# Optimization experiments

Measured on AMD Instinct MI355X. Metric: run time of the kernel, lower is better.

Reference implementation:

```python
import jax, jax.numpy as jnp
import numpy as np


def _slim_scale(out_c, wvec, dtype):
    # SlimConv2d splits output channels at 0.6/0.7/0.8/0.9 and scales splits 1..4
    # by weights[1..4] (split 0 is unscaled). Equivalent to one conv + channel scale.
    c0, c1, c2, c3 = int(0.6 * out_c), int(0.7 * out_c), int(0.8 * out_c), int(0.9 * out_c)
    return jnp.concatenate([
        jnp.ones((c0,), dtype),
        wvec[1] * jnp.ones((c1 - c0,), dtype),
        wvec[2] * jnp.ones((c2 - c1,), dtype),
        wvec[3] * jnp.ones((c3 - c2,), dtype),
        wvec[4] * jnp.ones((out_c - c3,), dtype),
    ])


def _slim_conv(x, W, b, pad_t, wvec):
    # x: (N,C,T,V), W: (O,I,kT,kV)
    y = jax.lax.conv_general_dilated(
        x, W, window_strides=(1, 1), padding=((pad_t, pad_t), (0, 0)),
        dimension_numbers=('NCHW', 'OIHW', 'NCHW'))
    y = y + b[None, :, None, None]
    scale = _slim_scale(W.shape[0], wvec, x.dtype)
    return y * scale[None, :, None, None]


def setup_inputs() -> dict:
    key = jax.random.key(0)
    ks = jax.random.split(key, 8)
    N, C, T, V = 64, 64, 300, 25
    S, IC = 3, 16  # num_subset, inter_channels = 64 // 4
    x = jax.random.normal(ks[0], (N, C, T, V), jnp.float32)
    weights = jax.random.uniform(ks[1], (5,), jnp.float32)
    A = jax.random.uniform(ks[2], (S, V, V), jnp.float32) * 0.1
    PA = jnp.full((S, V, V), 1e-6, jnp.float32)
    Wd = jax.random.normal(ks[3], (S, C, C, 1, 1), jnp.float32) * (2.0 / (C * 3)) ** 0.5
    bd = jnp.zeros((S, C), jnp.float32)
    WT1 = jax.random.normal(ks[4], (S, IC, C, 9, 1), jnp.float32) * 0.05
    bT1 = jnp.zeros((S, IC), jnp.float32)
    WT2 = jax.random.normal(ks[5], (S, IC, C, 9, 1), jnp.float32) * 0.05
    bT2 = jnp.zeros((S, IC), jnp.float32)
    bn_gamma = jnp.ones((C,), jnp.float32)
    bn_beta = jnp.zeros((C,), jnp.float32)
    bn_mean = jnp.zeros((C,), jnp.float32)
    bn_var = jnp.ones((C,), jnp.float32)
    return dict(x=x, weights=weights, A=A, PA=PA, Wd=Wd, bd=bd, WT1=WT1, bT1=bT1,
                WT2=WT2, bT2=bT2, bn_gamma=bn_gamma, bn_beta=bn_beta,
                bn_mean=bn_mean, bn_var=bn_var)


def reference(x, weights, A, PA, Wd, bd, WT1, bT1, WT2, bT2,
              bn_gamma, bn_beta, bn_mean, bn_var):
    N, C, T, V = x.shape
    inter_c = WT1.shape[1]
    num_subset = A.shape[0]
    # Chebyshev-like adjacency term: 8A^4 - 4A^2 - 4A + I (elementwise powers)
    A_ch = 8 * A ** 4 - 4 * A ** 2 - 4 * A + jnp.eye(V, dtype=A.dtype)
    A_full = A + PA + A_ch  # (S, V, V)
    y = None
    for i in range(num_subset):
        t1 = _slim_conv(x, WT1[i], bT1[i], 4, weights)  # (N, inter_c, T, V)
        t2 = _slim_conv(x, WT2[i], bT2[i], 4, weights)  # (N, inter_c, T, V)
        q = t1.transpose(0, 3, 1, 2).reshape(N, V, inter_c * T)  # (N, V, IC*T)
        k = t2.reshape(N, inter_c * T, V)                          # (N, IC*T, V)
        att = jax.nn.softmax(jnp.matmul(q, k) / (inter_c * T), axis=-2)  # (N, V, V)
        A1 = A_full[i] + att
        agg = jnp.matmul(x.reshape(N, C * T, V), A1).reshape(N, C, T, V)
        z = _slim_conv(agg, Wd[i], bd[i], 0, weights)
        y = z if y is None else y + z
    # BatchNorm2d in eval mode
    inv = jax.lax.rsqrt(bn_var + 1e-5)
    y = (y - bn_mean[None, :, None, None]) * (bn_gamma * inv)[None, :, None, None] \
        + bn_beta[None, :, None, None]
    y = y + x  # down is identity since in_channels == out_channels
    return jax.nn.relu(y)
```

## Files before the change

### kernel.cpp

```cpp
#include <hip/hip_runtime.h>

constexpr int N_ = 64, C_ = 64, T_ = 300, V_ = 25, IC_ = 16, S_ = 3, KT_ = 9;

constexpr int TTM   = 16;
constexpr int SROWS = TTM + 8;
constexpr int MROWS = SROWS * V_;
constexpr int CSTR  = 40;
constexpr int NTB   = (T_ + TTM - 1) / TTM;
constexpr int KS_   = 264;

constexpr int TTZ   = 16;
constexpr int NTBZ  = (T_ + TTZ - 1) / TTZ;
constexpr int ASTR  = 36;

typedef __bf16 bf16x8 __attribute__((ext_vector_type(8)));
typedef __bf16 bf16x4 __attribute__((ext_vector_type(4)));
typedef float  f32x4  __attribute__((ext_vector_type(4)));

constexpr int OFF_AFULL = 0;
constexpr int SZ_AFULL  = S_ * V_ * V_;
constexpr int OFF_WTB   = OFF_AFULL + SZ_AFULL;
constexpr int SZ_WTB_F  = (S_ * KT_ * 32 * C_) / 2;
constexpr int OFF_BTC   = OFF_WTB + SZ_WTB_F;
constexpr int OFF_WDB   = OFF_BTC + S_ * 32;
constexpr int SZ_WDB_F  = (S_ * C_ * C_) / 2;
constexpr int OFF_BDT   = OFF_WDB + SZ_WDB_F;
constexpr int OFF_BNA   = OFF_BDT + C_;
constexpr int OFF_BNB   = OFF_BNA + C_;
constexpr int OFF_A1    = OFF_BNB + C_;
constexpr int SZ_A1     = S_ * N_ * V_ * V_;
constexpr int OFF_SPART = OFF_A1 + SZ_A1;
constexpr int SZ_SPART  = S_ * N_ * NTB * V_ * V_;

__device__ __forceinline__ float slim16(const float* w, int o) {
    if (o < 9)  return 1.0f;
    if (o < 11) return w[1];
    if (o < 12) return w[2];
    if (o < 14) return w[3];
    return w[4];
}
__device__ __forceinline__ float slim64(const float* w, int o) {
    if (o < 38) return 1.0f;
    if (o < 44) return w[1];
    if (o < 51) return w[2];
    if (o < 57) return w[3];
    return w[4];
}

__global__ void prep_kernel(const float* __restrict__ wv,  const float* __restrict__ A,
                            const float* __restrict__ PA,  const float* __restrict__ Wd,
                            const float* __restrict__ bd,  const float* __restrict__ WT1,
                            const float* __restrict__ bT1, const float* __restrict__ WT2,
                            const float* __restrict__ bT2, const float* __restrict__ gam,
                            const float* __restrict__ bet, const float* __restrict__ mu,
                            const float* __restrict__ var, float* __restrict__ ws)
{
    const int gid = blockIdx.x * blockDim.x + threadIdx.x;
    const int stride = gridDim.x * blockDim.x;
    for (int idx = gid; idx < S_ * V_ * V_; idx += stride) {
        int uv = idx % (V_ * V_);
        int u = uv / V_, v = uv % V_;
        float a  = A[idx];
        float a2 = a * a;
        ws[OFF_AFULL + idx] = a + PA[idx] + 8.f * a2 * a2 - 4.f * a2 - 4.f * a
                              + (u == v ? 1.f : 0.f);
    }
    {
        __bf16* wtb = (__bf16*)(ws + OFF_WTB);
        for (int idx = gid; idx < S_ * KT_ * 32 * C_; idx += stride) {
            int c  = idx % C_;
            int r  = idx / C_;
            int o  = r % 32;  r /= 32;
            int kt = r % KT_;
            int i  = r / KT_;
            float val;
            if (o < IC_)
                val = slim16(wv, o) * WT1[((i * IC_ + o) * C_ + c) * KT_ + kt];
            else
                val = slim16(wv, o - IC_) * WT2[((i * IC_ + (o - IC_)) * C_ + c) * KT_ + kt];
            wtb[idx] = (__bf16)val;
        }
    }
    for (int idx = gid; idx < S_ * 32; idx += stride) {
        int i = idx / 32, o = idx % 32;
        float val = (o < IC_) ? slim16(wv, o) * bT1[i * IC_ + o]
                              : slim16(wv, o - IC_) * bT2[i * IC_ + (o - IC_)];
        ws[OFF_BTC + idx] = val;
    }
    {
        __bf16* wdb = (__bf16*)(ws + OFF_WDB);
        for (int idx = gid; idx < S_ * C_ * C_; idx += stride) {
            int c = idx % C_;
            int o = (idx / C_) % C_;
            int i = idx / (C_ * C_);
            wdb[idx] = (__bf16)(slim64(wv, o) * Wd[(i * C_ + o) * C_ + c]);
        }
    }
    for (int idx = gid; idx < C_; idx += stride) {
        float bt = 0.f;
        for (int i = 0; i < S_; ++i) bt += slim64(wv, idx) * bd[i * C_ + idx];
        ws[OFF_BDT + idx] = bt;
        float ba = gam[idx] * rsqrtf(var[idx] + 1e-5f);
        ws[OFF_BNA + idx] = ba;
        ws[OFF_BNB + idx] = bet[idx] - mu[idx] * ba;
    }
}

__global__ __launch_bounds__(320) void tconv_att_kernel(
    const float* __restrict__ x,  const __bf16* __restrict__ wt,
    const float* __restrict__ btc, float* __restrict__ spart)
{
    __shared__ __align__(16) char lds_raw[MROWS * CSTR * 2];
    __bf16* xs  = (__bf16*)lds_raw;
    __bf16* t1L = (__bf16*)lds_raw;
    __bf16* t2L = t1L + 32 * KS_;
    const int tid  = threadIdx.x;
    const int n    = blockIdx.y;
    const int tb   = blockIdx.x;
    const int t0   = tb * TTM;
    const int wv   = tid >> 6;
    const int lane = tid & 63;
    const int l15  = lane & 15;
    const int quad = lane >> 4;

    f32x4 acc[5][6];
#pragma unroll
    for (int j = 0; j < 5; ++j)
#pragma unroll
        for (int p = 0; p < 6; ++p) acc[j][p] = (f32x4){0.f, 0.f, 0.f, 0.f};

    for (int ch = 0; ch < 2; ++ch) {
        const int c0 = ch * 32;
        __syncthreads();
        for (int idx = tid; idx < MROWS * 4; idx += 320) {
            const int lr = idx % MROWS;
            const int cg = idx / MROWS;
            const int tg = t0 - 4 + lr / V_;
            bf16x8 pk;
            if (tg >= 0 && tg < T_) {
                const float* gp = x + ((size_t)(n * C_ + c0 + cg * 8) * T_ + (t0 - 4)) * V_ + lr;
#pragma unroll
                for (int jj = 0; jj < 8; ++jj) pk[jj] = (__bf16)gp[(size_t)jj * T_ * V_];
            } else {
#pragma unroll
                for (int jj = 0; jj < 8; ++jj) pk[jj] = (__bf16)0.f;
            }
            *(bf16x8*)&xs[lr * CSTR + cg * 8] = pk;
        }
        __syncthreads();

        for (int kt = 0; kt < KT_; ++kt) {
            bf16x8 a[6];
#pragma unroll
            for (int p = 0; p < 6; ++p) {
                const int i = p >> 1, h = p & 1;
                a[p] = *(const bf16x8*)&wt[((size_t)((i * KT_ + kt) * 32 + h * 16 + l15)) * C_ + c0 + quad * 8];
            }
#pragma unroll
            for (int j = 0; j < 5; ++j) {
                const int r = (wv * 5 + j) * 16 + l15 + V_ * kt;
                const bf16x8 b = *(const bf16x8*)&xs[r * CSTR + quad * 8];
#pragma unroll
                for (int p = 0; p < 6; ++p)
                    acc[j][p] = __builtin_amdgcn_mfma_f32_16x16x32_bf16(a[p], b, acc[j][p], 0, 0, 0);
            }
        }
    }

    for (int i = 0; i < S_; ++i) {
        __syncthreads();
#pragma unroll
        for (int j = 0; j < 5; ++j) {
            const int m  = (wv * 5 + j) * 16 + l15;
            const int tl = m / V_;
            const int u  = m % V_;
            const bool valid = (t0 + tl) < T_;
#pragma unroll
            for (int h = 0; h < 2; ++h) {
                const int p = i * 2 + h;
                __bf16* dst = h ? t2L : t1L;
#pragma unroll
                for (int r = 0; r < 4; ++r) {
                    const int o = quad * 4 + r;
                    const float val = valid ? (acc[j][p][r] + btc[i * 32 + h * 16 + o]) : 0.f;
                    dst[u * KS_ + o * 16 + tl] = (__bf16)val;
                }
            }
        }
        __syncthreads();
        if (wv < 4) {
            const int ut = wv >> 1, vt = wv & 1;
            f32x4 sa = (f32x4){0.f, 0.f, 0.f, 0.f};
#pragma unroll
            for (int ks = 0; ks < 8; ++ks) {
                const bf16x8 A = *(const bf16x8*)&t1L[(ut * 16 + l15) * KS_ + ks * 32 + quad * 8];
                const bf16x8 B = *(const bf16x8*)&t2L[(vt * 16 + l15) * KS_ + ks * 32 + quad * 8];
                sa = __builtin_amdgcn_mfma_f32_16x16x32_bf16(A, B, sa, 0, 0, 0);
            }
            float* sp = spart + (((size_t)i * N_ + n) * NTB + tb) * (V_ * V_);
#pragma unroll
            for (int r = 0; r < 4; ++r) {
                const int u = ut * 16 + quad * 4 + r;
                const int v = vt * 16 + l15;
                if (u < V_ && v < V_) sp[u * V_ + v] = sa[r];
            }
        }
    }
}

__global__ __launch_bounds__(256) void att_softmax_kernel(
    const float* __restrict__ spart, const float* __restrict__ afull,
    float* __restrict__ a1o)
{
    __shared__ float Ss[V_ * V_];
    const int n = blockIdx.x;
    const int i = blockIdx.y;
    const int tid = threadIdx.x;
    for (int p = tid; p < V_ * V_; p += 256) {
        float s = 0.f;
        const float* sp = spart + (((size_t)i * N_ + n) * NTB) * (V_ * V_) + p;
        for (int blk = 0; blk < NTB; ++blk)
            s += sp[(size_t)blk * (V_ * V_)];
        Ss[p] = s * (1.0f / (IC_ * T_));
    }
    __syncthreads();
    if (tid < V_) {
        const int v = tid;
        float m = -1e30f;
#pragma unroll
        for (int u = 0; u < V_; ++u) m = fmaxf(m, Ss[u * V_ + v]);
        float e[V_]; float es = 0.f;
#pragma unroll
        for (int u = 0; u < V_; ++u) { e[u] = expf(Ss[u * V_ + v] - m); es += e[u]; }
        const float inv = 1.0f / es;
#pragma unroll
        for (int u = 0; u < V_; ++u)
            a1o[((size_t)i * N_ + n) * (V_ * V_) + u * V_ + v]
                = afull[i * (V_ * V_) + u * V_ + v] + e[u] * inv;
    }
}

__global__ __launch_bounds__(320) void agg_out_mfma_kernel(
    const float* __restrict__ x,   const float* __restrict__ a1,
    const __bf16* __restrict__ wdb, const float* __restrict__ bdt,
    const float* __restrict__ bna, const float* __restrict__ bnb,
    float* __restrict__ out)
{
    __shared__ __align__(16) __bf16 ags[400 * ASTR];
    __shared__ __align__(16) __bf16 a1t3[S_ * 32 * 32];
    const int tid  = threadIdx.x;
    const int n    = blockIdx.y;
    const int t0   = blockIdx.x * TTZ;
    const int wv   = tid >> 6;
    const int lane = tid & 63;
    const int l15  = lane & 15;
    const int quad = lane >> 4;

    for (int idx = tid; idx < S_ * 1024; idx += 320) {
        const int i = idx >> 10;
        const int r = idx & 1023;
        const int v = r >> 5, u = r & 31;
        float val = (v < V_ && u < V_)
                  ? a1[((size_t)(i * N_ + n) * V_ + u) * V_ + v] : 0.f;
        a1t3[idx] = (__bf16)val;
    }

    f32x4 acc[5][4];
#pragma unroll
    for (int j = 0; j < 5; ++j)
#pragma unroll
        for (int ot = 0; ot < 4; ++ot) acc[j][ot] = (f32x4){0.f, 0.f, 0.f, 0.f};

    const int tg = t0 + l15;
    for (int chunk = 0; chunk < 2; ++chunk) {
        const int c0 = chunk * 32;
        bf16x8 afr[7];
#pragma unroll
        for (int k = 0; k < 7; ++k) {
            const int c = wv + 5 * k;
            bf16x8 pk;
#pragma unroll
            for (int jj = 0; jj < 8; ++jj) pk[jj] = (__bf16)0.f;
            if (c < 32 && tg < T_) {
                const float* gp = x + ((size_t)(n * C_ + c0 + c) * T_ + tg) * V_;
#pragma unroll
                for (int jj = 0; jj < 8; ++jj) {
                    const int u = quad * 8 + jj;
                    if (u < V_) pk[jj] = (__bf16)gp[u];
                }
            }
            afr[k] = pk;
        }
        for (int i = 0; i < S_; ++i) {
            __syncthreads();
            const bf16x8 b0 = *(const bf16x8*)&a1t3[i * 1024 + l15 * 32 + quad * 8];
            const bf16x8 b1 = *(const bf16x8*)&a1t3[i * 1024 + (16 + l15) * 32 + quad * 8];
#pragma unroll
            for (int k = 0; k < 7; ++k) {
                const int c = wv + 5 * k;
                if (c < 32) {
                    f32x4 d0 = (f32x4){0.f, 0.f, 0.f, 0.f};
                    f32x4 d1 = (f32x4){0.f, 0.f, 0.f, 0.f};
                    d0 = __builtin_amdgcn_mfma_f32_16x16x32_bf16(afr[k], b0, d0, 0, 0, 0);
                    d1 = __builtin_amdgcn_mfma_f32_16x16x32_bf16(afr[k], b1, d1, 0, 0, 0);
#pragma unroll
                    for (int r = 0; r < 4; ++r) {
                        const int tl = quad * 4 + r;
                        ags[(tl * V_ + l15) * ASTR + c] = (__bf16)d0[r];
                        if (l15 < V_ - 16)
                            ags[(tl * V_ + 16 + l15) * ASTR + c] = (__bf16)d1[r];
                    }
                }
            }
            __syncthreads();
            bf16x8 bw[4];
#pragma unroll
            for (int ot = 0; ot < 4; ++ot)
                bw[ot] = *(const bf16x8*)&wdb[(size_t)(i * C_ + ot * 16 + l15) * C_ + c0 + quad * 8];
#pragma unroll
            for (int j = 0; j < 5; ++j) {
                const int m2 = (wv * 5 + j) * 16 + l15;
                const bf16x4 lo = *(const bf16x4*)&ags[m2 * ASTR + quad * 8];
                const bf16x4 hi = *(const bf16x4*)&ags[m2 * ASTR + quad * 8 + 4];
                const bf16x8 am = __builtin_shufflevector(lo, hi, 0, 1, 2, 3, 4, 5, 6, 7);
#pragma unroll
                for (int ot = 0; ot < 4; ++ot)
                    acc[j][ot] = __builtin_amdgcn_mfma_f32_16x16x32_bf16(am, bw[ot], acc[j][ot], 0, 0, 0);
            }
        }
    }

    const int mrem = (T_ - t0) * V_;
#pragma unroll
    for (int ot = 0; ot < 4; ++ot) {
        const int o  = ot * 16 + l15;
        const float ba = bna[o], bb = bnb[o], bt = bdt[o];
#pragma unroll
        for (int j = 0; j < 5; ++j) {
            const int m2b = (wv * 5 + j) * 16 + quad * 4;
            if (m2b + 3 < mrem) {
                const size_t gi = (size_t)(n * C_ + o) * (T_ * V_) + (size_t)t0 * V_ + m2b;
                const f32x4 xr = *(const f32x4*)&x[gi];
                f32x4 rs;
#pragma unroll
                for (int r = 0; r < 4; ++r)
                    rs[r] = fmaxf(fmaf(acc[j][ot][r] + bt, ba, bb) + xr[r], 0.f);
                *(f32x4*)&out[gi] = rs;
            }
        }
    }
}

extern "C" void kernel_launch(void* const* d_in, const int* in_sizes, int n_in,
                              void* d_out, int out_size, void* d_ws, size_t ws_size,
                              hipStream_t stream)
{
    (void)in_sizes; (void)n_in; (void)out_size; (void)ws_size;
    const float* x    = (const float*)d_in[0];
    const float* wv   = (const float*)d_in[1];
    const float* A    = (const float*)d_in[2];
    const float* PA   = (const float*)d_in[3];
    const float* Wd   = (const float*)d_in[4];
    const float* bd   = (const float*)d_in[5];
    const float* WT1  = (const float*)d_in[6];
    const float* bT1  = (const float*)d_in[7];
    const float* WT2  = (const float*)d_in[8];
    const float* bT2  = (const float*)d_in[9];
    const float* gam  = (const float*)d_in[10];
    const float* bet  = (const float*)d_in[11];
    const float* mu   = (const float*)d_in[12];
    const float* var  = (const float*)d_in[13];
    float* ws  = (float*)d_ws;
    float* out = (float*)d_out;

    prep_kernel<<<dim3(64), dim3(256), 0, stream>>>(
        wv, A, PA, Wd, bd, WT1, bT1, WT2, bT2, gam, bet, mu, var, ws);

    tconv_att_kernel<<<dim3(NTB, N_), dim3(320), 0, stream>>>(
        x, (const __bf16*)(ws + OFF_WTB), ws + OFF_BTC, ws + OFF_SPART);

    att_softmax_kernel<<<dim3(N_, S_), dim3(256), 0, stream>>>(
        ws + OFF_SPART, ws + OFF_AFULL, ws + OFF_A1);

    agg_out_mfma_kernel<<<dim3(NTBZ, N_), dim3(320), 0, stream>>>(
        x, ws + OFF_A1, (const __bf16*)(ws + OFF_WDB),
        ws + OFF_BDT, ws + OFF_BNA, ws + OFF_BNB, out);
}
```

Baseline: 552.0 us.

## Retile temporal conv to 12 steps with swizzled LDS and atomic score accumulation

Shrinks the time tile of the temporal conv/attention kernel from 16 to 12 so it divides T exactly. This removes padded rows and boundary checks, and 300 tile rows map onto 19 MFMA tiles spread across waves. The LDS channel stride drops to 32 with an XOR swizzle to avoid bank conflicts, and t1/t2 are written as packed 4-element vectors. Per-block partial attention scores are accumulated with global atomicAdd into a zeroed buffer instead of a partial array that softmax reduces later. The trade-off is more blocks and atomic contention, plus an order-dependent floating-point sum.

```diff
diff --git a/kernel.cpp b/kernel.cpp
--- a/kernel.cpp
+++ b/kernel.cpp
@@ -2,12 +2,14 @@
 
 constexpr int N_ = 64, C_ = 64, T_ = 300, V_ = 25, IC_ = 16, S_ = 3, KT_ = 9;
 
-constexpr int TTM   = 16;
+constexpr int TTM   = 12;
 constexpr int SROWS = TTM + 8;
 constexpr int MROWS = SROWS * V_;
-constexpr int CSTR  = 40;
-constexpr int NTB   = (T_ + TTM - 1) / TTM;
-constexpr int KS_   = 264;
+constexpr int XROWS = MROWS + 4;
+constexpr int CSTR  = 32;
+constexpr int NTB   = T_ / TTM;
+constexpr int NTILE = (TTM * V_ + 15) / 16;
+constexpr int KS_   = 204;
 
 constexpr int TTZ   = 16;
 constexpr int NTBZ  = (T_ + TTZ - 1) / TTZ;
@@ -29,8 +31,8 @@
 constexpr int OFF_BNB   = OFF_BNA + C_;
 constexpr int OFF_A1    = OFF_BNB + C_;
 constexpr int SZ_A1     = S_ * N_ * V_ * V_;
-constexpr int OFF_SPART = OFF_A1 + SZ_A1;
-constexpr int SZ_SPART  = S_ * N_ * NTB * V_ * V_;
+constexpr int OFF_SACC  = OFF_A1 + SZ_A1;
+constexpr int SZ_SACC   = S_ * N_ * V_ * V_;
 
 __device__ __forceinline__ float slim16(const float* w, int o) {
     if (o < 9)  return 1.0f;
@@ -57,6 +59,8 @@
 {
     const int gid = blockIdx.x * blockDim.x + threadIdx.x;
     const int stride = gridDim.x * blockDim.x;
+    for (int idx = gid; idx < SZ_SACC; idx += stride)
+        ws[OFF_SACC + idx] = 0.f;
     for (int idx = gid; idx < S_ * V_ * V_; idx += stride) {
         int uv = idx % (V_ * V_);
         int u = uv / V_, v = uv % V_;
@@ -108,24 +112,30 @@
 
 __global__ __launch_bounds__(320) void tconv_att_kernel(
     const float* __restrict__ x,  const __bf16* __restrict__ wt,
-    const float* __restrict__ btc, float* __restrict__ spart)
-{
-    __shared__ __align__(16) char lds_raw[MROWS * CSTR * 2];
+    const float* __restrict__ btc, float* __restrict__ sacc)
+{
+    __shared__ __align__(16) char lds_raw[XROWS * CSTR * 2];
     __bf16* xs  = (__bf16*)lds_raw;
     __bf16* t1L = (__bf16*)lds_raw;
     __bf16* t2L = t1L + 32 * KS_;
     const int tid  = threadIdx.x;
     const int n    = blockIdx.y;
-    const int tb   = blockIdx.x;
-    const int t0   = tb * TTM;
+    const int t0   = blockIdx.x * TTM;
     const int wv   = tid >> 6;
     const int lane = tid & 63;
     const int l15  = lane & 15;
     const int quad = lane >> 4;
 
-    f32x4 acc[5][6];
-#pragma unroll
-    for (int j = 0; j < 5; ++j)
+    if (tid < 16) {
+        bf16x8 z;
+#pragma unroll
+        for (int jj = 0; jj < 8; ++jj) z[jj] = (__bf16)0.f;
+        *(bf16x8*)&xs[(MROWS + (tid >> 2)) * CSTR + (tid & 3) * 8] = z;
+    }
+
+    f32x4 acc[4][6];
+#pragma unroll
+    for (int j = 0; j < 4; ++j)
 #pragma unroll
         for (int p = 0; p < 6; ++p) acc[j][p] = (f32x4){0.f, 0.f, 0.f, 0.f};
 
@@ -145,7 +155,7 @@
 #pragma unroll
                 for (int jj = 0; jj < 8; ++jj) pk[jj] = (__bf16)0.f;
             }
-            *(bf16x8*)&xs[lr * CSTR + cg * 8] = pk;
+            *(bf16x8*)&xs[lr * CSTR + ((cg ^ (lr & 3)) << 3)] = pk;
         }
         __syncthreads();
 
@@ -157,12 +167,15 @@
                 a[p] = *(const bf16x8*)&wt[((size_t)((i * KT_ + kt) * 32 + h * 16 + l15)) * C_ + c0 + quad * 8];
             }
 #pragma unroll
-            for (int j = 0; j < 5; ++j) {
-                const int r = (wv * 5 + j) * 16 + l15 + V_ * kt;
-                const bf16x8 b = *(const bf16x8*)&xs[r * CSTR + quad * 8];
-#pragma unroll
-                for (int p = 0; p < 6; ++p)
-                    acc[j][p] = __builtin_amdgcn_mfma_f32_16x16x32_bf16(a[p], b, acc[j][p], 0, 0, 0);
+            for (int j = 0; j < 4; ++j) {
+                const int jt = wv + 5 * j;
+                if (jt < NTILE) {
+                    const int r = jt * 16 + l15 + V_ * kt;
+                    const bf16x8 b = *(const bf16x8*)&xs[r * CSTR + ((quad ^ (r & 3)) << 3)];
+#pragma unroll
+                    for (int p = 0; p < 6; ++p)
+                        acc[j][p] = __builtin_amdgcn_mfma_f32_16x16x32_bf16(a[p], b, acc[j][p], 0, 0, 0);
+                }
             }
         }
     }
@@ -170,20 +183,22 @@
     for (int i = 0; i < S_; ++i) {
         __syncthreads();
 #pragma unroll
-        for (int j = 0; j < 5; ++j) {
-            const int m  = (wv * 5 + j) * 16 + l15;
-            const int tl = m / V_;
-            const int u  = m % V_;
-            const bool valid = (t0 + tl) < T_;
-#pragma unroll
-            for (int h = 0; h < 2; ++h) {
-                const int p = i * 2 + h;
-                __bf16* dst = h ? t2L : t1L;
-#pragma unroll
-                for (int r = 0; r < 4; ++r) {
-                    const int o = quad * 4 + r;
-                    const float val = valid ? (acc[j][p][r] + btc[i * 32 + h * 16 + o]) : 0.f;
-                    dst[u * KS_ + o * 16 + tl] = (__bf16)val;
+        for (int j = 0; j < 4; ++j) {
+            const int jt = wv + 5 * j;
+            if (jt < NTILE) {
+                const int m = jt * 16 + l15;
+                if (m < TTM * V_) {
+                    const int tl = m / V_;
+                    const int u  = m % V_;
+#pragma unroll
+                    for (int h = 0; h < 2; ++h) {
+                        bf16x4 pk;
+#pragma unroll
+                        for (int r = 0; r < 4; ++r)
+                            pk[r] = (__bf16)(acc[j][i * 2 + h][r] + btc[i * 32 + h * 16 + quad * 4 + r]);
+                        __bf16* dst = (h ? t2L : t1L) + u * KS_ + tl * 16 + quad * 4;
+                        *(bf16x4*)dst = pk;
+                    }
                 }
             }
         }
@@ -192,37 +207,32 @@
             const int ut = wv >> 1, vt = wv & 1;
             f32x4 sa = (f32x4){0.f, 0.f, 0.f, 0.f};
 #pragma unroll
-            for (int ks = 0; ks < 8; ++ks) {
+            for (int ks = 0; ks < 6; ++ks) {
                 const bf16x8 A = *(const bf16x8*)&t1L[(ut * 16 + l15) * KS_ + ks * 32 + quad * 8];
                 const bf16x8 B = *(const bf16x8*)&t2L[(vt * 16 + l15) * KS_ + ks * 32 + quad * 8];
                 sa = __builtin_amdgcn_mfma_f32_16x16x32_bf16(A, B, sa, 0, 0, 0);
             }
-            float* sp = spart + (((size_t)i * N_ + n) * NTB + tb) * (V_ * V_);
+            float* sp = sacc + ((size_t)i * N_ + n) * (V_ * V_);
 #pragma unroll
             for (int r = 0; r < 4; ++r) {
                 const int u = ut * 16 + quad * 4 + r;
                 const int v = vt * 16 + l15;
-                if (u < V_ && v < V_) sp[u * V_ + v] = sa[r];
+                if (u < V_ && v < V_) atomicAdd(&sp[u * V_ + v], sa[r]);
             }
         }
     }
 }
 
 __global__ __launch_bounds__(256) void att_softmax_kernel(
-    const float* __restrict__ spart, const float* __restrict__ afull,
+    const float* __restrict__ sacc, const float* __restrict__ afull,
     float* __restrict__ a1o)
 {
     __shared__ float Ss[V_ * V_];
     const int n = blockIdx.x;
     const int i = blockIdx.y;
     const int tid = threadIdx.x;
-    for (int p = tid; p < V_ * V_; p += 256) {
-        float s = 0.f;
-        const float* sp = spart + (((size_t)i * N_ + n) * NTB) * (V_ * V_) + p;
-        for (int blk = 0; blk < NTB; ++blk)
-            s += sp[(size_t)blk * (V_ * V_)];
-        Ss[p] = s * (1.0f / (IC_ * T_));
-    }
+    for (int p = tid; p < V_ * V_; p += 256)
+        Ss[p] = sacc[((size_t)i * N_ + n) * (V_ * V_) + p] * (1.0f / (IC_ * T_));
     __syncthreads();
     if (tid < V_) {
         const int v = tid;
@@ -377,10 +387,10 @@
         wv, A, PA, Wd, bd, WT1, bT1, WT2, bT2, gam, bet, mu, var, ws);
 
     tconv_att_kernel<<<dim3(NTB, N_), dim3(320), 0, stream>>>(
-        x, (const __bf16*)(ws + OFF_WTB), ws + OFF_BTC, ws + OFF_SPART);
+        x, (const __bf16*)(ws + OFF_WTB), ws + OFF_BTC, ws + OFF_SACC);
 
     att_softmax_kernel<<<dim3(N_, S_), dim3(256), 0, stream>>>(
-        ws + OFF_SPART, ws + OFF_AFULL, ws + OFF_A1);
+        ws + OFF_SACC, ws + OFF_AFULL, ws + OFF_A1);
 
     agg_out_mfma_kernel<<<dim3(NTBZ, N_), dim3(320), 0, stream>>>(
         x, ws + OFF_A1, (const __bf16*)(ws + OFF_WDB),
```

New measurement: 598.2 us. +8.4%, slower.

## Pre-transpose x to padded bf16 channel-last layout and atomically accumulate attention scores

Applied to the files above, without the earlier changes.

Adds a pass in the prep kernel that converts x once into a time-padded, channel-last bf16 tensor, stored in the output buffer as scratch. The temporal-conv kernel can then load its LDS tiles with contiguous 16-byte reads instead of strided fp32 gathers with bounds checks. Per-block attention partials are now summed straight into a small accumulator with float atomics, so the softmax kernel no longer reduces over all time blocks. The t1/t2 LDS writes are packed into bf16x4 stores with a changed layout and padding. Costs are an extra full pass over x, a much larger prep grid, atomic contention, and order-dependent float summation.

```diff
diff --git a/kernel.cpp b/kernel.cpp
--- a/kernel.cpp
+++ b/kernel.cpp
@@ -1,13 +1,15 @@
 #include <hip/hip_runtime.h>
 
 constexpr int N_ = 64, C_ = 64, T_ = 300, V_ = 25, IC_ = 16, S_ = 3, KT_ = 9;
+
+constexpr int TP_   = T_ + 12;
 
 constexpr int TTM   = 16;
 constexpr int SROWS = TTM + 8;
 constexpr int MROWS = SROWS * V_;
-constexpr int CSTR  = 40;
+constexpr int CSTR  = 32;
 constexpr int NTB   = (T_ + TTM - 1) / TTM;
-constexpr int KS_   = 264;
+constexpr int KS_   = 266;
 
 constexpr int TTZ   = 16;
 constexpr int NTBZ  = (T_ + TTZ - 1) / TTZ;
@@ -29,8 +31,8 @@
 constexpr int OFF_BNB   = OFF_BNA + C_;
 constexpr int OFF_A1    = OFF_BNB + C_;
 constexpr int SZ_A1     = S_ * N_ * V_ * V_;
-constexpr int OFF_SPART = OFF_A1 + SZ_A1;
-constexpr int SZ_SPART  = S_ * N_ * NTB * V_ * V_;
+constexpr int OFF_SACC  = OFF_A1 + SZ_A1;
+constexpr int SZ_SACC   = S_ * N_ * V_ * V_;
 
 __device__ __forceinline__ float slim16(const float* w, int o) {
     if (o < 9)  return 1.0f;
@@ -47,7 +49,8 @@
     return w[4];
 }
 
-__global__ void prep_kernel(const float* __restrict__ wv,  const float* __restrict__ A,
+__global__ void prep_kernel(const float* __restrict__ x,   __bf16* __restrict__ xt,
+                            const float* __restrict__ wv,  const float* __restrict__ A,
                             const float* __restrict__ PA,  const float* __restrict__ Wd,
                             const float* __restrict__ bd,  const float* __restrict__ WT1,
                             const float* __restrict__ bT1, const float* __restrict__ WT2,
@@ -57,6 +60,25 @@
 {
     const int gid = blockIdx.x * blockDim.x + threadIdx.x;
     const int stride = gridDim.x * blockDim.x;
+    for (int idx = gid; idx < N_ * TP_ * V_ * 8; idx += stride) {
+        const int cg = idx & 7;
+        const int v  = (idx >> 3) % V_;
+        const int tt = (idx / (V_ * 8)) % TP_;
+        const int n  = idx / (V_ * 8 * TP_);
+        const int t  = tt - 4;
+        bf16x8 pk;
+        if (t >= 0 && t < T_) {
+            const float* gp = x + ((size_t)(n * C_ + cg * 8) * T_ + t) * V_ + v;
+#pragma unroll
+            for (int jj = 0; jj < 8; ++jj) pk[jj] = (__bf16)gp[(size_t)jj * T_ * V_];
+        } else {
+#pragma unroll
+            for (int jj = 0; jj < 8; ++jj) pk[jj] = (__bf16)0.f;
+        }
+        *(bf16x8*)&xt[((size_t)(n * TP_ + tt) * V_ + v) * C_ + cg * 8] = pk;
+    }
+    for (int idx = gid; idx < SZ_SACC; idx += stride)
+        ws[OFF_SACC + idx] = 0.f;
     for (int idx = gid; idx < S_ * V_ * V_; idx += stride) {
         int uv = idx % (V_ * V_);
         int u = uv / V_, v = uv % V_;
@@ -107,8 +129,8 @@
 }
 
 __global__ __launch_bounds__(320) void tconv_att_kernel(
-    const float* __restrict__ x,  const __bf16* __restrict__ wt,
-    const float* __restrict__ btc, float* __restrict__ spart)
+    const __bf16* __restrict__ xt, const __bf16* __restrict__ wt,
+    const float* __restrict__ btc, float* __restrict__ sacc)
 {
     __shared__ __align__(16) char lds_raw[MROWS * CSTR * 2];
     __bf16* xs  = (__bf16*)lds_raw;
@@ -116,8 +138,7 @@
     __bf16* t2L = t1L + 32 * KS_;
     const int tid  = threadIdx.x;
     const int n    = blockIdx.y;
-    const int tb   = blockIdx.x;
-    const int t0   = tb * TTM;
+    const int t0   = blockIdx.x * TTM;
     const int wv   = tid >> 6;
     const int lane = tid & 63;
     const int l15  = lane & 15;
@@ -132,20 +153,13 @@
     for (int ch = 0; ch < 2; ++ch) {
         const int c0 = ch * 32;
         __syncthreads();
-        for (int idx = tid; idx < MROWS * 4; idx += 320) {
-            const int lr = idx % MROWS;
-            const int cg = idx / MROWS;
-            const int tg = t0 - 4 + lr / V_;
-            bf16x8 pk;
-            if (tg >= 0 && tg < T_) {
-                const float* gp = x + ((size_t)(n * C_ + c0 + cg * 8) * T_ + (t0 - 4)) * V_ + lr;
-#pragma unroll
-                for (int jj = 0; jj < 8; ++jj) pk[jj] = (__bf16)gp[(size_t)jj * T_ * V_];
-            } else {
-#pragma unroll
-                for (int jj = 0; jj < 8; ++jj) pk[jj] = (__bf16)0.f;
-            }
-            *(bf16x8*)&xs[lr * CSTR + cg * 8] = pk;
+        {
+            const __bf16* xtb = xt + (size_t)(n * TP_ + t0) * (V_ * C_) + c0;
+            for (int idx = tid; idx < MROWS * 4; idx += 320) {
+                const int lr = idx >> 2, cg = idx & 3;
+                const bf16x8 pk = *(const bf16x8*)&xtb[lr * C_ + cg * 8];
+                *(bf16x8*)&xs[idx * 8] = pk;
+            }
         }
         __syncthreads();
 
@@ -177,14 +191,15 @@
             const bool valid = (t0 + tl) < T_;
 #pragma unroll
             for (int h = 0; h < 2; ++h) {
-                const int p = i * 2 + h;
-                __bf16* dst = h ? t2L : t1L;
+                bf16x4 pk;
 #pragma unroll
                 for (int r = 0; r < 4; ++r) {
-                    const int o = quad * 4 + r;
-                    const float val = valid ? (acc[j][p][r] + btc[i * 32 + h * 16 + o]) : 0.f;
-                    dst[u * KS_ + o * 16 + tl] = (__bf16)val;
+                    const float val = valid
+                        ? (acc[j][i * 2 + h][r] + btc[i * 32 + h * 16 + quad * 4 + r])
+                        : 0.f;
+                    pk[r] = (__bf16)val;
                 }
+                *(bf16x4*)((h ? t2L : t1L) + u * KS_ + tl * 16 + quad * 4) = pk;
             }
         }
         __syncthreads();
@@ -197,32 +212,27 @@
                 const bf16x8 B = *(const bf16x8*)&t2L[(vt * 16 + l15) * KS_ + ks * 32 + quad * 8];
                 sa = __builtin_amdgcn_mfma_f32_16x16x32_bf16(A, B, sa, 0, 0, 0);
             }
-            float* sp = spart + (((size_t)i * N_ + n) * NTB + tb) * (V_ * V_);
+            float* sp = sacc + ((size_t)i * N_ + n) * (V_ * V_);
 #pragma unroll
             for (int r = 0; r < 4; ++r) {
                 const int u = ut * 16 + quad * 4 + r;
                 const int v = vt * 16 + l15;
-                if (u < V_ && v < V_) sp[u * V_ + v] = sa[r];
+                if (u < V_ && v < V_) atomicAdd(&sp[u * V_ + v], sa[r]);
             }
         }
     }
 }
 
 __global__ __launch_bounds__(256) void att_softmax_kernel(
-    const float* __restrict__ spart, const float* __restrict__ afull,
+    const float* __restrict__ sacc, const float* __restrict__ afull,
     float* __restrict__ a1o)
 {
     __shared__ float Ss[V_ * V_];
     const int n = blockIdx.x;
     const int i = blockIdx.y;
     const int tid = threadIdx.x;
-    for (int p = tid; p < V_ * V_; p += 256) {
-        float s = 0.f;
-        const float* sp = spart + (((size_t)i * N_ + n) * NTB) * (V_ * V_) + p;
-        for (int blk = 0; blk < NTB; ++blk)
-            s += sp[(size_t)blk * (V_ * V_)];
-        Ss[p] = s * (1.0f / (IC_ * T_));
-    }
+    for (int p = tid; p < V_ * V_; p += 256)
+        Ss[p] = sacc[((size_t)i * N_ + n) * (V_ * V_) + p] * (1.0f / (IC_ * T_));
     __syncthreads();
     if (tid < V_) {
         const int v = tid;
@@ -373,14 +383,16 @@
     float* ws  = (float*)d_ws;
     float* out = (float*)d_out;
 
-    prep_kernel<<<dim3(64), dim3(256), 0, stream>>>(
-        wv, A, PA, Wd, bd, WT1, bT1, WT2, bT2, gam, bet, mu, var, ws);
+    __bf16* xt = (__bf16*)d_out;
+
+    prep_kernel<<<dim3(15600), dim3(256), 0, stream>>>(
+        x, xt, wv, A, PA, Wd, bd, WT1, bT1, WT2, bT2, gam, bet, mu, var, ws);
 
     tconv_att_kernel<<<dim3(NTB, N_), dim3(320), 0, stream>>>(
-        x, (const __bf16*)(ws + OFF_WTB), ws + OFF_BTC, ws + OFF_SPART);
+        xt, (const __bf16*)(ws + OFF_WTB), ws + OFF_BTC, ws + OFF_SACC);
 
     att_softmax_kernel<<<dim3(N_, S_), dim3(256), 0, stream>>>(
-        ws + OFF_SPART, ws + OFF_AFULL, ws + OFF_A1);
+        ws + OFF_SACC, ws + OFF_AFULL, ws + OFF_A1);
 
     agg_out_mfma_kernel<<<dim3(NTBZ, N_), dim3(320), 0, stream>>>(
         x, ws + OFF_A1, (const __bf16*)(ws + OFF_WDB),
```

Result: slower. 568.8 us (+3.0%).
